# Optimization experiments

Hardware: AMD Instinct MI355X
Metric: run time of the kernel (lower is better)

## Reference

```python
import jax, jax.numpy as jnp
import numpy as np
from functools import partial

EMB = 768
ATTN = 768
HEADS = 12
N = 4096
K = 64
ALPHA = 0.5
TEMP = 0.5
THRESH = 1e-4
MAX_ITER = 100
DKM_EPS = 1e-6
LN_EPS = 1e-5


def setup_inputs() -> dict:
    key = jax.random.key(0)
    ks = jax.random.split(key, 12)
    s = 0.02
    return {
        "original_embeddings": jax.random.normal(ks[0], (N, EMB), jnp.float32),
        "fc1_w": jax.random.normal(ks[1], (ATTN, EMB), jnp.float32) * s,
        "fc1_b": jnp.zeros((ATTN,), jnp.float32),
        "fc2_w": jax.random.normal(ks[2], (EMB, ATTN), jnp.float32) * s,
        "fc2_b": jnp.zeros((EMB,), jnp.float32),
        "in_proj_w": jax.random.normal(ks[3], (3 * ATTN, ATTN), jnp.float32) * s,
        "in_proj_b": jnp.zeros((3 * ATTN,), jnp.float32),
        "out_w": jax.random.normal(ks[4], (ATTN, ATTN), jnp.float32) * s,
        "out_b": jnp.zeros((ATTN,), jnp.float32),
        "ln_g": jnp.ones((EMB,), jnp.float32),
        "ln_b": jnp.zeros((EMB,), jnp.float32),
        "init_idx": jax.random.randint(ks[5], (K,), 0, N, jnp.int64 if jax.config.jax_enable_x64 else jnp.int32),
        "k_cl": K,
    }


def _cdist(x, c):
    # squared euclidean via expansion, clipped for numerical safety
    sq = (jnp.sum(x * x, 1)[:, None] + jnp.sum(c * c, 1)[None, :]
          - 2.0 * (x @ c.T))
    return jnp.sqrt(jnp.maximum(sq, 0.0))


def _dkm_step(X, C):
    a = jax.nn.softmax(-_cdist(X, C) / TEMP, axis=1)   # [N, K]
    a_sum = jnp.sum(a, axis=0) + DKM_EPS               # [K]
    C_new = (a.T @ X) / a_sum[:, None]                 # [K, D]
    return a, C_new


def _transform(x, fc1_w, fc1_b, fc2_w, fc2_b, in_proj_w, in_proj_b, out_w, out_b, ln_g, ln_b):
    h = jax.nn.relu(x @ fc1_w.T + fc1_b)               # [N, A]
    qkv = h @ in_proj_w.T + in_proj_b                  # [N, 3A]
    q, k, v = jnp.split(qkv, 3, axis=1)
    hd = ATTN // HEADS
    q = q.reshape(N, HEADS, hd).transpose(1, 0, 2)     # [H, N, hd]
    k = k.reshape(N, HEADS, hd).transpose(1, 0, 2)
    v = v.reshape(N, HEADS, hd).transpose(1, 0, 2)
    scores = jnp.einsum('hnd,hmd->hnm', q, k) / np.sqrt(hd).astype(np.float32)
    attn = jax.nn.softmax(scores, axis=-1)             # [H, N, N]
    o = jnp.einsum('hnm,hmd->hnd', attn, v)            # [H, N, hd]
    o = o.transpose(1, 0, 2).reshape(N, ATTN)
    o = o @ out_w.T + out_b
    y = jax.nn.relu(o @ fc2_w.T + fc2_b)               # [N, E]
    z = (1.0 - ALPHA) * x + ALPHA * y
    mu = jnp.mean(z, axis=-1, keepdims=True)
    var = jnp.mean((z - mu) ** 2, axis=-1, keepdims=True)
    return (z - mu) / jnp.sqrt(var + LN_EPS) * ln_g + ln_b


def reference(original_embeddings, fc1_w, fc1_b, fc2_w, fc2_b,
              in_proj_w, in_proj_b, out_w, out_b, ln_g, ln_b,
              init_idx, k_cl):
    X = _transform(original_embeddings, fc1_w, fc1_b, fc2_w, fc2_b,
                   in_proj_w, in_proj_b, out_w, out_b, ln_g, ln_b)
    C0 = X[init_idx]                                   # [K, E]
    a0, C1 = _dkm_step(X, C0)
    diff0 = jnp.sum(jnp.abs(C1 - C0))

    def cond(st):
        _, _, _, diff, i = st
        return (diff > THRESH) & (i < MAX_ITER)

    def body(st):
        _, _, C_new, _, i = st
        C = C_new
        a, C_new2 = _dkm_step(X, C)
        diff = jnp.sum(jnp.abs(C_new2 - C))
        return (C, a, C_new2, diff, i + 1)

    C, a, _, _, _ = jax.lax.while_loop(cond, body, (C0, a0, C1, diff0, jnp.int32(0)))
    return C, a
```

## Files before the change

### kernel.cpp

```cpp
#include <hip/hip_runtime.h>
#include <cstdint>

typedef __bf16 bf16;
typedef __bf16 bf16x4 __attribute__((ext_vector_type(4)));
typedef __bf16 bf16x8 __attribute__((ext_vector_type(8)));
typedef float  f32x4  __attribute__((ext_vector_type(4)));

#define LOG2E 1.44269504088896340736f

__device__ __forceinline__ f32x4 mfma16(bf16x8 a, bf16x8 b, f32x4 c) {
  return __builtin_amdgcn_mfma_f32_16x16x32_bf16(a, b, c, 0, 0, 0);
}

__device__ __forceinline__ void gl2lds16(const bf16* g, bf16* l) {
  __builtin_amdgcn_global_load_lds(
      (const __attribute__((address_space(1))) unsigned int*)g,
      (__attribute__((address_space(3))) unsigned int*)l, 16, 0, 0);
}

__global__ __launch_bounds__(256) void cvt_all(
    const float* __restrict__ x0, const float* __restrict__ w1,
    const float* __restrict__ w2, const float* __restrict__ wip,
    const float* __restrict__ wo,
    bf16* __restrict__ dx0, bf16* __restrict__ dw1, bf16* __restrict__ dw2,
    bf16* __restrict__ dwip, bf16* __restrict__ dwo, float* __restrict__ ctrl)
{
  int i = blockIdx.x * 256 + threadIdx.x;
  if (blockIdx.x == 0) {
    for (int u = threadIdx.x; u < 8192; u += 256) ctrl[u] = 0.f;
  }
  const float* s; bf16* d; int base;
  if      (i <  786432) { s = x0;  d = dx0;  base = 0; }
  else if (i <  933888) { s = w1;  d = dw1;  base = 786432; }
  else if (i < 1081344) { s = w2;  d = dw2;  base = 933888; }
  else if (i < 1523712) { s = wip; d = dwip; base = 1081344; }
  else                  { s = wo;  d = dwo;  base = 1523712; }
  int j = i - base;
  f32x4 v = ((const f32x4*)s)[j];
  bf16x4 r;
  r[0] = (bf16)v[0]; r[1] = (bf16)v[1]; r[2] = (bf16)v[2]; r[3] = (bf16)v[3];
  ((bf16x4*)d)[j] = r;
}

template<int RELU, int OUTF32>
__global__ __launch_bounds__(256) void gemm128(
    const bf16* __restrict__ A, const bf16* __restrict__ W,
    const float* __restrict__ bias, bf16* __restrict__ outb,
    float* __restrict__ outf, int N)
{
  __shared__ bf16 Ab[2][8192];
  __shared__ bf16 Bb[2][8192];
  const int tid = threadIdx.x;
  const int w = tid >> 6, lane = tid & 63;
  const int q2 = lane >> 4, c = lane & 15;
  const int wrow = (w >> 1) * 64, wcol = (w & 1) * 64;
  const int mb = blockIdx.x * 128, nb = blockIdx.y * 128;
  const int srow = tid >> 3, sgrp = tid & 7;

  auto stage = [&](const bf16* __restrict__ src, int rowbase, int kb, bf16* dst) {
#pragma unroll
    for (int i = 0; i < 4; ++i) {
      int row = i * 32 + srow;
      int gs = (sgrp ^ (row & 7)) * 8;
      gl2lds16(src + (size_t)(rowbase + row) * 768 + kb + gs,
               dst + i * 2048 + tid * 8);
    }
  };

  f32x4 acc[4][4] = {};
  stage(A, mb, 0, Ab[0]);
  stage(W, nb, 0, Bb[0]);
  for (int kb = 0; kb < 12; ++kb) {
    const int buf = kb & 1;
    __syncthreads();
    if (kb < 11) {
      stage(A, mb, (kb + 1) * 64, Ab[buf ^ 1]);
      stage(W, nb, (kb + 1) * 64, Bb[buf ^ 1]);
    }
#pragma unroll
    for (int kc = 0; kc < 2; ++kc) {
      bf16x8 af[4], bfr[4];
#pragma unroll
      for (int rt = 0; rt < 4; ++rt) {
        int r = wrow + rt * 16 + c;
        af[rt] = *(const bf16x8*)&Ab[buf][r * 64 + (((kc * 4 + q2) ^ (r & 7)) * 8)];
      }
#pragma unroll
      for (int ct = 0; ct < 4; ++ct) {
        int r = wcol + ct * 16 + c;
        bfr[ct] = *(const bf16x8*)&Bb[buf][r * 64 + (((kc * 4 + q2) ^ (r & 7)) * 8)];
      }
#pragma unroll
      for (int rt = 0; rt < 4; ++rt)
#pragma unroll
        for (int ct = 0; ct < 4; ++ct)
          acc[rt][ct] = mfma16(af[rt], bfr[ct], acc[rt][ct]);
    }
  }
#pragma unroll
  for (int rt = 0; rt < 4; ++rt) {
#pragma unroll
    for (int ct = 0; ct < 4; ++ct) {
      int col = nb + wcol + ct * 16 + c;
      float bv = bias[col];
#pragma unroll
      for (int j = 0; j < 4; ++j) {
        int row = mb + wrow + rt * 16 + q2 * 4 + j;
        float v = acc[rt][ct][j] + bv;
        if (RELU) v = fmaxf(v, 0.f);
        if (OUTF32) outf[(size_t)row * N + col] = v;
        else        outb[(size_t)row * N + col] = (bf16)v;
      }
    }
  }
}

__global__ __launch_bounds__(256) void transpose_bf16(
    const bf16* __restrict__ src, bf16* __restrict__ dst, int stride, int colOff)
{
  __shared__ bf16 t[64][72];
  const int br = blockIdx.x, bc = blockIdx.y;
  {
    int ir = threadIdx.x >> 2, icb = (threadIdx.x & 3) * 16;
    const bf16* srow = src + (size_t)(br * 64 + ir) * stride + colOff + bc * 64 + icb;
    *(bf16x8*)&t[ir][icb] = *(const bf16x8*)srow;
    *(bf16x8*)&t[ir][icb + 8] = *(const bf16x8*)(srow + 8);
  }
  __syncthreads();
  {
    int oc = threadIdx.x >> 2, orb = (threadIdx.x & 3) * 16;
    bf16x8 v0, v1;
#pragma unroll
    for (int j = 0; j < 8; ++j) { v0[j] = t[orb + j][oc]; v1[j] = t[orb + 8 + j][oc]; }
    bf16* drow = dst + (size_t)(bc * 64 + oc) * 4096 + br * 64 + orb;
    *(bf16x8*)drow = v0;
    *(bf16x8*)(drow + 8) = v1;
  }
}

__global__ __launch_bounds__(256) void attn_kernel(
    const bf16* __restrict__ qkv, const bf16* __restrict__ vt, bf16* __restrict__ o)
{
  const int h = blockIdx.x >> 6;
  const int qt = blockIdx.x & 63;
  const int w = threadIdx.x >> 6, lane = threadIdx.x & 63;
  const int q2 = lane >> 4, c = lane & 15;
  const int qbase = qt * 64 + w * 16;
  __shared__ bf16 Ks[2][64][64];
  __shared__ bf16 Vs[2][64][64];
  __shared__ bf16 Pl[4][16][72];

  const bf16* Qr = qkv + (size_t)(qbase + c) * 2304 + h * 64 + q2 * 8;
  bf16x8 a0 = *(const bf16x8*)(Qr);
  bf16x8 a1 = *(const bf16x8*)(Qr + 32);

  const int srow = lane >> 3;
  const int sg = ((lane & 7) ^ srow) * 8;
  const bf16* kg = qkv + (size_t)(w * 16 + srow) * 2304 + 768 + h * 64 + sg;
  const bf16* vg = vt + (size_t)(h * 64 + w * 16 + srow) * 4096 + sg;

  auto stage = [&](int jt, int buf) {
    const int kvb = jt * 64;
    gl2lds16(kg + (size_t)kvb * 2304,       &Ks[buf][w * 16][0]);
    gl2lds16(kg + (size_t)(kvb + 8) * 2304, &Ks[buf][w * 16 + 8][0]);
    gl2lds16(vg + kvb,                      &Vs[buf][w * 16][0]);
    gl2lds16(vg + kvb + 8 * 4096,           &Vs[buf][w * 16 + 8][0]);
  };

  bf16x8 ones;
#pragma unroll
  for (int i = 0; i < 8; ++i) ones[i] = (bf16)1.0f;

  f32x4 oa[4] = {};
  f32x4 accl = {};
  const int gsw = (q2 ^ (c & 7)) * 8;
  const float SC = 0.125f * LOG2E;

  stage(0, 0);
  for (int jt = 0; jt < 64; ++jt) {
    const int buf = jt & 1;
    __syncthreads();
    if (jt < 63) stage(jt + 1, buf ^ 1);
    f32x4 s[4];
#pragma unroll
    for (int nt = 0; nt < 4; ++nt) {
      const int row = nt * 16 + c;
      bf16x8 b0 = *(const bf16x8*)&Ks[buf][row][gsw];
      bf16x8 b1 = *(const bf16x8*)&Ks[buf][row][gsw ^ 32];
      f32x4 t = {};
      t = mfma16(a0, b0, t);
      t = mfma16(a1, b1, t);
      s[nt] = t;
    }
#pragma unroll
    for (int nt = 0; nt < 4; ++nt)
#pragma unroll
      for (int j = 0; j < 4; ++j)
        Pl[w][q2 * 4 + j][nt * 16 + c] = (bf16)exp2f(s[nt][j] * SC);
    bf16x8 p0 = *(const bf16x8*)(&Pl[w][c][q2 * 8]);
    bf16x8 p1 = *(const bf16x8*)(&Pl[w][c][32 + q2 * 8]);
    accl = mfma16(p0, ones, accl);
    accl = mfma16(p1, ones, accl);
#pragma unroll
    for (int dt = 0; dt < 4; ++dt) {
      const int row = dt * 16 + c;
      bf16x8 v0 = *(const bf16x8*)&Vs[buf][row][gsw];
      bf16x8 v1 = *(const bf16x8*)&Vs[buf][row][gsw ^ 32];
      oa[dt] = mfma16(p0, v0, oa[dt]);
      oa[dt] = mfma16(p1, v1, oa[dt]);
    }
  }
#pragma unroll
  for (int dt = 0; dt < 4; ++dt)
#pragma unroll
    for (int j = 0; j < 4; ++j) {
      int row = qbase + q2 * 4 + j;
      int col = h * 64 + dt * 16 + c;
      o[(size_t)row * 768 + col] = (bf16)(oa[dt][j] / accl[j]);
    }
}

__global__ __launch_bounds__(256) void ln_kernel(
    const float* __restrict__ x0, const float* __restrict__ y,
    const float* __restrict__ g, const float* __restrict__ b,
    float* __restrict__ X, bf16* __restrict__ Xb, float* __restrict__ xn2)
{
  const int w = threadIdx.x >> 6, lane = threadIdx.x & 63;
  const int row = blockIdx.x * 4 + w;
  const float* xr = x0 + (size_t)row * 768;
  const float* yr = y + (size_t)row * 768;
  float z[12]; float s = 0.f;
#pragma unroll
  for (int i = 0; i < 12; ++i) {
    int col = lane + i * 64;
    float zz = 0.5f * xr[col] + 0.5f * yr[col];
    z[i] = zz; s += zz;
  }
#pragma unroll
  for (int off = 32; off; off >>= 1) s += __shfl_xor(s, off, 64);
  float mu = s * (1.f / 768.f);
  float v = 0.f;
#pragma unroll
  for (int i = 0; i < 12; ++i) { float d = z[i] - mu; v += d * d; }
#pragma unroll
  for (int off = 32; off; off >>= 1) v += __shfl_xor(v, off, 64);
  float rstd = rsqrtf(v * (1.f / 768.f) + 1e-5f);
  float sn = 0.f;
#pragma unroll
  for (int i = 0; i < 12; ++i) {
    int col = lane + i * 64;
    float xv = (z[i] - mu) * rstd * g[col] + b[col];
    X[(size_t)row * 768 + col] = xv;
    Xb[(size_t)row * 768 + col] = (bf16)xv;
    sn += xv * xv;
  }
#pragma unroll
  for (int off = 32; off; off >>= 1) sn += __shfl_xor(sn, off, 64);
  if (lane == 0) xn2[row] = sn;
}

__device__ __forceinline__ void gridbar(int* bar, int& ep, int g) {
  __syncthreads();
  if (threadIdx.x == 0) {
    ep++;
    __builtin_amdgcn_fence(__ATOMIC_RELEASE, "agent");
    int v = __hip_atomic_fetch_add(bar + g * 64, 1, __ATOMIC_RELAXED,
                                   __HIP_MEMORY_SCOPE_AGENT) + 1;
    if (v == 32 * ep) {
      int tv = __hip_atomic_fetch_add(bar + 512, 1, __ATOMIC_RELAXED,
                                      __HIP_MEMORY_SCOPE_AGENT) + 1;
      if (tv == 8 * ep) {
#pragma unroll
        for (int i = 0; i < 8; ++i)
          __hip_atomic_store(bar + 1024 + i * 64, ep, __ATOMIC_RELAXED,
                             __HIP_MEMORY_SCOPE_AGENT);
      }
    }
    long guard = 0;
    while (__hip_atomic_load(bar + 1024 + g * 64, __ATOMIC_RELAXED,
                             __HIP_MEMORY_SCOPE_AGENT) < ep) {
      __builtin_amdgcn_s_sleep(2);
      if (++guard > (1L << 28)) break;
    }
    __builtin_amdgcn_fence(__ATOMIC_ACQUIRE, "agent");
  }
  __syncthreads();
}

__global__ __launch_bounds__(256) void dkm_fused(
    const float* __restrict__ XF, const int* __restrict__ idx,
    const bf16* __restrict__ Xb, const bf16* __restrict__ Xt,
    const float* __restrict__ xn2,
    float* __restrict__ CB, bf16* __restrict__ CBH,
    bf16* __restrict__ aT, float* __restrict__ a_out, float* __restrict__ outC,
    float* __restrict__ asumall, float* __restrict__ cnall,
    float* __restrict__ diffall, int* __restrict__ bar)
{
  extern __shared__ char dynsmem[];
  bf16* XtL = (bf16*)dynsmem;
  __shared__ bf16 XL[16][776];
  __shared__ float GsRed[1024];
  __shared__ float asl[64];
  __shared__ float cnl[16];
  __shared__ float dred[4];
  __shared__ float sdiff;
  float (*Gs)[64] = (float(*)[64])GsRed;
  float (*red)[16][16] = (float(*)[16][16])GsRed;
  const int tid = threadIdx.x;
  const int w = tid >> 6, lane = tid & 63;
  const int q2 = lane >> 4, c = lane & 15;
  const int b = blockIdx.x;
  const int g = b & 7;
  const int rbase = b * 16;
  const int tr = b / 48, tc = b % 48;
  int ep = 0;

  {
    int row = tid >> 4, seg = (tid & 15) * 48;
    const bf16* src = Xb + (size_t)(rbase + row) * 768 + seg;
#pragma unroll
    for (int i = 0; i < 6; ++i)
      *(bf16x8*)&XL[row][seg + i * 8] = *(const bf16x8*)(src + i * 8);
  }
  if (b < 192) {
    const int row = tid >> 4, cc = tid & 15;
    const bf16* XtS = Xt + (size_t)(tc * 16 + row) * 4096;
#pragma unroll
    for (int i = 0; i < 32; ++i) {
      int gg = i * 16 + cc;
      bf16x8 vv = *(const bf16x8*)(XtS + gg * 8);
      *(bf16x8*)&XtL[(size_t)row * 4096 + ((gg ^ (row & 7)) * 8)] = vv;
    }
  }
  if (b < 64) {
    const int src = idx[b];
    float s = 0.f;
#pragma unroll
    for (int u = 0; u < 3; ++u) {
      int d = u * 256 + tid;
      float v = XF[(size_t)src * 768 + d];
      CB[(size_t)b * 768 + d] = v;
      CBH[(size_t)b * 768 + d] = (bf16)v;
      s += v * v;
    }
#pragma unroll
    for (int off = 32; off; off >>= 1) s += __shfl_xor(s, off, 64);
    if (lane == 0) dred[w] = s;
    __syncthreads();
    if (tid == 0) cnall[b] = dred[0] + dred[1] + dred[2] + dred[3];
  }
  const int arow = tid >> 4, aci = tid & 15;
  const float xn = xn2[rbase + arow];
  gridbar(bar, ep, g);

  int p = 0;
  for (int t = 0; t < 100; ++t) {
    const int par = t & 1;
    {
      if (b == 0) {
        if (tid >= 128 && tid < 192) asumall[(par ^ 1) * 64 + tid - 128] = 0.f;
        else if (tid >= 192)         cnall[(par ^ 1) * 64 + tid - 192] = 0.f;
      }
      const bf16* C = CBH + (size_t)par * 49152;
      const float* cnp = cnall + par * 64;
      f32x4 acc = {};
      const bf16* Cr = C + (size_t)(w * 16 + c) * 768 + q2 * 8;
#pragma unroll
      for (int ks = 0; ks < 24; ++ks) {
        bf16x8 a = *(const bf16x8*)&XL[c][q2 * 8 + ks * 32];
        bf16x8 bb = *(const bf16x8*)(Cr + ks * 32);
        acc = mfma16(a, bb, acc);
      }
      if (tid < 64) asl[tid] = 0.f;
#pragma unroll
      for (int j = 0; j < 4; ++j) Gs[q2 * 4 + j][w * 16 + c] = acc[j];
      __syncthreads();
      float lg[4];
#pragma unroll
      for (int u = 0; u < 4; ++u) {
        int col = aci + u * 16;
        float d2 = xn + cnp[col] - 2.f * Gs[arow][col];
        lg[u] = -2.f * sqrtf(fmaxf(d2, 0.f));
      }
      float mx = fmaxf(fmaxf(lg[0], lg[1]), fmaxf(lg[2], lg[3]));
#pragma unroll
      for (int off = 8; off; off >>= 1) mx = fmaxf(mx, __shfl_xor(mx, off, 16));
      float sum = 0.f;
#pragma unroll
      for (int u = 0; u < 4; ++u) { float e = exp2f((lg[u] - mx) * LOG2E); lg[u] = e; sum += e; }
#pragma unroll
      for (int off = 8; off; off >>= 1) sum += __shfl_xor(sum, off, 16);
      float rs = 1.f / sum;
#pragma unroll
      for (int u = 0; u < 4; ++u) {
        int col = aci + u * 16;
        float av = lg[u] * rs;
        aT[(size_t)col * 4096 + rbase + arow] = (bf16)av;
        atomicAdd(&asl[col], av);
      }
      __syncthreads();
      if (tid < 64) atomicAdd(&asumall[par * 64 + tid], asl[tid]);
    }
    gridbar(bar, ep, g);
    if (b < 192) {
      f32x4 acc = {};
      const bf16* Ar = aT + (size_t)(tr * 16 + c) * 4096 + q2 * 8;
#pragma unroll 4
      for (int i = 0; i < 32; ++i) {
        int kb = (w + i * 4) * 32;
        int gb = (w + i * 4) * 4 + q2;
        bf16x8 bv = *(const bf16x8*)&XtL[(size_t)c * 4096 + ((gb ^ (c & 7)) * 8)];
        acc = mfma16(*(const bf16x8*)(Ar + kb), bv, acc);
      }
#pragma unroll
      for (int j = 0; j < 4; ++j) red[w][q2 * 4 + j][c] = acc[j];
      if (tid < 16) cnl[tid] = 0.f;
      __syncthreads();
      const int r = tid >> 4, cl = tid & 15;
      float s = red[0][r][cl] + red[1][r][cl] + red[2][r][cl] + red[3][r][cl];
      const int cluster = tr * 16 + r, dcol = tc * 16 + cl;
      float denom = asumall[par * 64 + cluster] + 1e-6f;
      float cnew = s / denom;
      size_t cidx = (size_t)cluster * 768 + dcol;
      float cold = CB[(size_t)par * 49152 + cidx];
      CB[(size_t)(par ^ 1) * 49152 + cidx] = cnew;
      CBH[(size_t)(par ^ 1) * 49152 + cidx] = (bf16)cnew;
      atomicAdd(&cnl[r], cnew * cnew);
      float dv = fabsf(cnew - cold);
#pragma unroll
      for (int off = 32; off; off >>= 1) dv += __shfl_xor(dv, off, 64);
      if (lane == 0) dred[w] = dv;
      __syncthreads();
      if (tid < 16)
        atomicAdd(&cnall[(par ^ 1) * 64 + tr * 16 + tid], cnl[tid]);
      if (tid == 0)
        atomicAdd(&diffall[par], dred[0] + dred[1] + dred[2] + dred[3]);
    } else if (b == 255 && tid == 0) {
      diffall[par ^ 1] = 0.f;
    }
    gridbar(bar, ep, g);
    if (tid == 0)
      sdiff = *(volatile const float*)&diffall[par];
    __syncthreads();
    if (sdiff <= 1e-4f) { p = par; break; }
    p = (t + 1) & 1;
  }
  {
    const bf16* C = CBH + (size_t)p * 49152;
    const float* cnp = cnall + p * 64;
    f32x4 acc = {};
    const bf16* Cr = C + (size_t)(w * 16 + c) * 768 + q2 * 8;
#pragma unroll
    for (int ks = 0; ks < 24; ++ks) {
      bf16x8 a = *(const bf16x8*)&XL[c][q2 * 8 + ks * 32];
      bf16x8 bb = *(const bf16x8*)(Cr + ks * 32);
      acc = mfma16(a, bb, acc);
    }
    __syncthreads();
#pragma unroll
    for (int j = 0; j < 4; ++j) Gs[q2 * 4 + j][w * 16 + c] = acc[j];
    __syncthreads();
    float lg[4];
#pragma unroll
    for (int u = 0; u < 4; ++u) {
      int col = aci + u * 16;
      float d2 = xn + cnp[col] - 2.f * Gs[arow][col];
      lg[u] = -2.f * sqrtf(fmaxf(d2, 0.f));
    }
    float mx = fmaxf(fmaxf(lg[0], lg[1]), fmaxf(lg[2], lg[3]));
#pragma unroll
    for (int off = 8; off; off >>= 1) mx = fmaxf(mx, __shfl_xor(mx, off, 16));
    float sum = 0.f;
#pragma unroll
    for (int u = 0; u < 4; ++u) { float e = exp2f((lg[u] - mx) * LOG2E); lg[u] = e; sum += e; }
#pragma unroll
    for (int off = 8; off; off >>= 1) sum += __shfl_xor(sum, off, 16);
    float rs = 1.f / sum;
#pragma unroll
    for (int u = 0; u < 4; ++u)
      a_out[(size_t)(rbase + arow) * 64 + aci + u * 16] = lg[u] * rs;
  }
  if (tid < 192) outC[b * 192 + tid] = CB[(size_t)p * 49152 + b * 192 + tid];
}

extern "C" void kernel_launch(void* const* d_in, const int* in_sizes, int n_in,
                              void* d_out, int out_size, void* d_ws, size_t ws_size,
                              hipStream_t stream) {
  const float* x0   = (const float*)d_in[0];
  const float* fc1w = (const float*)d_in[1];
  const float* fc1b = (const float*)d_in[2];
  const float* fc2w = (const float*)d_in[3];
  const float* fc2b = (const float*)d_in[4];
  const float* ipw  = (const float*)d_in[5];
  const float* ipb  = (const float*)d_in[6];
  const float* outw = (const float*)d_in[7];
  const float* outbias = (const float*)d_in[8];
  const float* lng  = (const float*)d_in[9];
  const float* lnb  = (const float*)d_in[10];
  const int*   idx  = (const int*)d_in[11];

  char* p = (char*)d_ws;
  auto take = [&](size_t n) { char* r = p; p += (n + 255) & ~(size_t)255; return r; };
  bf16* X0B   = (bf16*)take((size_t)4096 * 768 * 2);
  bf16* W1B   = (bf16*)take((size_t)768 * 768 * 2);
  bf16* FC2WB = (bf16*)take((size_t)768 * 768 * 2);
  bf16* IPWB  = (bf16*)take((size_t)2304 * 768 * 2);
  bf16* OUTWB = (bf16*)take((size_t)768 * 768 * 2);
  bf16* HB    = (bf16*)take((size_t)4096 * 768 * 2);
  bf16* QKVB  = (bf16*)take((size_t)4096 * 2304 * 2);
  bf16* VT    = (bf16*)take((size_t)768 * 4096 * 2);
  bf16* OB    = (bf16*)take((size_t)4096 * 768 * 2);
  bf16* O2B   = (bf16*)take((size_t)4096 * 768 * 2);
  float* YF   = (float*)take((size_t)4096 * 768 * 4);
  float* XF   = (float*)take((size_t)4096 * 768 * 4);
  bf16* XBB   = (bf16*)take((size_t)4096 * 768 * 2);
  bf16* XTB   = (bf16*)take((size_t)768 * 4096 * 2);
  float* XN2  = (float*)take((size_t)4096 * 4);
  float* CB   = (float*)take((size_t)2 * 49152 * 4);
  bf16* CBH   = (bf16*)take((size_t)2 * 49152 * 2);
  bf16* ATB   = (bf16*)take((size_t)64 * 4096 * 2);
  float* CTRLF = (float*)take(8192 * 4);
  float* ASUM = CTRLF;
  float* CN   = CTRLF + 128;
  float* DIFF = CTRLF + 256;
  int* BAR    = (int*)(CTRLF + 512);

  float* aout = (float*)d_out + 49152;

  cvt_all<<<6528, 256, 0, stream>>>(x0, fc1w, fc2w, ipw, outw,
                                    X0B, W1B, FC2WB, IPWB, OUTWB, CTRLF);
  gemm128<1, 0><<<dim3(32, 6), 256, 0, stream>>>(X0B, W1B, fc1b, HB, nullptr, 768);
  gemm128<0, 0><<<dim3(32, 18), 256, 0, stream>>>(HB, IPWB, ipb, QKVB, nullptr, 2304);
  transpose_bf16<<<dim3(64, 12), 256, 0, stream>>>(QKVB, VT, 2304, 1536);
  attn_kernel<<<768, 256, 0, stream>>>(QKVB, VT, OB);
  gemm128<0, 0><<<dim3(32, 6), 256, 0, stream>>>(OB, OUTWB, outbias, O2B, nullptr, 768);
  gemm128<1, 1><<<dim3(32, 6), 256, 0, stream>>>(O2B, FC2WB, fc2b, nullptr, YF, 768);
  ln_kernel<<<1024, 256, 0, stream>>>(x0, YF, lng, lnb, XF, XBB, XN2);
  transpose_bf16<<<dim3(64, 12), 256, 0, stream>>>(XBB, XTB, 768, 0);
  dkm_fused<<<256, 256, 131072, stream>>>(XF, idx, XBB, XTB, XN2, CB, CBH, ATB, aout,
                                          (float*)d_out, ASUM, CN, DIFF, BAR);
}
```

Measured before the change: 562.0 us.

## Fold out-proj into fc2 weights, widen attention KV tiles, split DKM accumulators

Precomputes the product of the fc2 and out-projection weights, plus a combined bias, so that one GEMM replaces two per-token GEMMs after attention. The attention kernel now stages 128-key tiles per iteration, halving the number of barriers and stage calls, with a new swizzle for the V tile. The DKM distance and centroid MFMA chains are split into four independent accumulators to shorten dependency chains. The folded weight product adds small setup kernels and an extra bf16 rounding of the combined weight, which may slightly change numerics.

```diff
diff --git a/kernel.cpp b/kernel.cpp
--- a/kernel.cpp
+++ b/kernel.cpp
@@ -42,6 +42,16 @@
   ((bf16x4*)d)[j] = r;
 }
 
+__global__ __launch_bounds__(256) void bias_fuse(
+    const float* __restrict__ w2, const float* __restrict__ bo,
+    const float* __restrict__ b2, float* __restrict__ bc)
+{
+  int n = blockIdx.x * 256 + threadIdx.x;
+  float s = 0.f;
+  for (int j = 0; j < 768; ++j) s += w2[(size_t)n * 768 + j] * bo[j];
+  bc[n] = b2[n] + s;
+}
+
 template<int RELU, int OUTF32>
 __global__ __launch_bounds__(256) void gemm128(
     const bf16* __restrict__ A, const bf16* __restrict__ W,
@@ -116,7 +126,8 @@
 }
 
 __global__ __launch_bounds__(256) void transpose_bf16(
-    const bf16* __restrict__ src, bf16* __restrict__ dst, int stride, int colOff)
+    const bf16* __restrict__ src, bf16* __restrict__ dst,
+    int stride, int colOff, int dstride)
 {
   __shared__ bf16 t[64][72];
   const int br = blockIdx.x, bc = blockIdx.y;
@@ -132,7 +143,7 @@
     bf16x8 v0, v1;
 #pragma unroll
     for (int j = 0; j < 8; ++j) { v0[j] = t[orb + j][oc]; v1[j] = t[orb + 8 + j][oc]; }
-    bf16* drow = dst + (size_t)(bc * 64 + oc) * 4096 + br * 64 + orb;
+    bf16* drow = dst + (size_t)(bc * 64 + oc) * dstride + br * 64 + orb;
     *(bf16x8*)drow = v0;
     *(bf16x8*)(drow + 8) = v1;
   }
@@ -146,25 +157,33 @@
   const int w = threadIdx.x >> 6, lane = threadIdx.x & 63;
   const int q2 = lane >> 4, c = lane & 15;
   const int qbase = qt * 64 + w * 16;
-  __shared__ bf16 Ks[2][64][64];
-  __shared__ bf16 Vs[2][64][64];
+  __shared__ bf16 Ks[2][128][64];
+  __shared__ bf16 Vs[2][64][128];
   __shared__ bf16 Pl[4][16][72];
 
   const bf16* Qr = qkv + (size_t)(qbase + c) * 2304 + h * 64 + q2 * 8;
   bf16x8 a0 = *(const bf16x8*)(Qr);
   bf16x8 a1 = *(const bf16x8*)(Qr + 32);
 
-  const int srow = lane >> 3;
-  const int sg = ((lane & 7) ^ srow) * 8;
-  const bf16* kg = qkv + (size_t)(w * 16 + srow) * 2304 + 768 + h * 64 + sg;
-  const bf16* vg = vt + (size_t)(h * 64 + w * 16 + srow) * 4096 + sg;
+  const int sr8 = lane >> 3, sc8 = lane & 7;
+  const int sr4 = lane >> 4, sc16 = lane & 15;
+  const int kcol = ((sc8 ^ sr8) * 8);
 
   auto stage = [&](int jt, int buf) {
-    const int kvb = jt * 64;
-    gl2lds16(kg + (size_t)kvb * 2304,       &Ks[buf][w * 16][0]);
-    gl2lds16(kg + (size_t)(kvb + 8) * 2304, &Ks[buf][w * 16 + 8][0]);
-    gl2lds16(vg + kvb,                      &Vs[buf][w * 16][0]);
-    gl2lds16(vg + kvb + 8 * 4096,           &Vs[buf][w * 16 + 8][0]);
+    const int kvb = jt * 128;
+#pragma unroll
+    for (int i = 0; i < 4; ++i) {
+      int rb = w * 32 + i * 8;
+      gl2lds16(qkv + (size_t)(kvb + rb + sr8) * 2304 + 768 + h * 64 + kcol,
+               &Ks[buf][rb][0]);
+    }
+#pragma unroll
+    for (int i = 0; i < 4; ++i) {
+      int rb = w * 16 + i * 4;
+      int key = i * 4 + sr4;
+      gl2lds16(vt + (size_t)(h * 64 + rb + sr4) * 4096 + kvb + (sc16 ^ key) * 8,
+               &Vs[buf][rb][0]);
+    }
   };
 
   bf16x8 ones;
@@ -177,37 +196,41 @@
   const float SC = 0.125f * LOG2E;
 
   stage(0, 0);
-  for (int jt = 0; jt < 64; ++jt) {
+  for (int jt = 0; jt < 32; ++jt) {
     const int buf = jt & 1;
     __syncthreads();
-    if (jt < 63) stage(jt + 1, buf ^ 1);
-    f32x4 s[4];
-#pragma unroll
-    for (int nt = 0; nt < 4; ++nt) {
-      const int row = nt * 16 + c;
-      bf16x8 b0 = *(const bf16x8*)&Ks[buf][row][gsw];
-      bf16x8 b1 = *(const bf16x8*)&Ks[buf][row][gsw ^ 32];
-      f32x4 t = {};
-      t = mfma16(a0, b0, t);
-      t = mfma16(a1, b1, t);
-      s[nt] = t;
-    }
-#pragma unroll
-    for (int nt = 0; nt < 4; ++nt)
-#pragma unroll
-      for (int j = 0; j < 4; ++j)
-        Pl[w][q2 * 4 + j][nt * 16 + c] = (bf16)exp2f(s[nt][j] * SC);
-    bf16x8 p0 = *(const bf16x8*)(&Pl[w][c][q2 * 8]);
-    bf16x8 p1 = *(const bf16x8*)(&Pl[w][c][32 + q2 * 8]);
-    accl = mfma16(p0, ones, accl);
-    accl = mfma16(p1, ones, accl);
-#pragma unroll
-    for (int dt = 0; dt < 4; ++dt) {
-      const int row = dt * 16 + c;
-      bf16x8 v0 = *(const bf16x8*)&Vs[buf][row][gsw];
-      bf16x8 v1 = *(const bf16x8*)&Vs[buf][row][gsw ^ 32];
-      oa[dt] = mfma16(p0, v0, oa[dt]);
-      oa[dt] = mfma16(p1, v1, oa[dt]);
+    if (jt < 31) stage(jt + 1, buf ^ 1);
+#pragma unroll
+    for (int half = 0; half < 2; ++half) {
+      f32x4 s[4];
+#pragma unroll
+      for (int nt = 0; nt < 4; ++nt) {
+        const int row = half * 64 + nt * 16 + c;
+        bf16x8 b0 = *(const bf16x8*)&Ks[buf][row][gsw];
+        bf16x8 b1 = *(const bf16x8*)&Ks[buf][row][gsw ^ 32];
+        f32x4 t = {};
+        t = mfma16(a0, b0, t);
+        t = mfma16(a1, b1, t);
+        s[nt] = t;
+      }
+#pragma unroll
+      for (int nt = 0; nt < 4; ++nt)
+#pragma unroll
+        for (int j = 0; j < 4; ++j)
+          Pl[w][q2 * 4 + j][nt * 16 + c] = (bf16)exp2f(s[nt][j] * SC);
+      bf16x8 p0 = *(const bf16x8*)(&Pl[w][c][q2 * 8]);
+      bf16x8 p1 = *(const bf16x8*)(&Pl[w][c][32 + q2 * 8]);
+      accl = mfma16(p0, ones, accl);
+      accl = mfma16(p1, ones, accl);
+      const int G0 = half * 8 + q2;
+#pragma unroll
+      for (int dt = 0; dt < 4; ++dt) {
+        const int row = dt * 16 + c;
+        bf16x8 v0 = *(const bf16x8*)&Vs[buf][row][(G0 ^ c) * 8];
+        bf16x8 v1 = *(const bf16x8*)&Vs[buf][row][((G0 + 4) ^ c) * 8];
+        oa[dt] = mfma16(p0, v0, oa[dt]);
+        oa[dt] = mfma16(p1, v1, oa[dt]);
+      }
     }
   }
 #pragma unroll
@@ -363,14 +386,20 @@
       }
       const bf16* C = CBH + (size_t)par * 49152;
       const float* cnp = cnall + par * 64;
-      f32x4 acc = {};
       const bf16* Cr = C + (size_t)(w * 16 + c) * 768 + q2 * 8;
-#pragma unroll
-      for (int ks = 0; ks < 24; ++ks) {
-        bf16x8 a = *(const bf16x8*)&XL[c][q2 * 8 + ks * 32];
-        bf16x8 bb = *(const bf16x8*)(Cr + ks * 32);
-        acc = mfma16(a, bb, acc);
-      }
+      f32x4 a0 = {}, a1 = {}, a2 = {}, a3 = {};
+#pragma unroll
+      for (int ks = 0; ks < 24; ks += 4) {
+        a0 = mfma16(*(const bf16x8*)&XL[c][q2 * 8 + ks * 32],
+                    *(const bf16x8*)(Cr + ks * 32), a0);
+        a1 = mfma16(*(const bf16x8*)&XL[c][q2 * 8 + (ks + 1) * 32],
+                    *(const bf16x8*)(Cr + (ks + 1) * 32), a1);
+        a2 = mfma16(*(const bf16x8*)&XL[c][q2 * 8 + (ks + 2) * 32],
+                    *(const bf16x8*)(Cr + (ks + 2) * 32), a2);
+        a3 = mfma16(*(const bf16x8*)&XL[c][q2 * 8 + (ks + 3) * 32],
+                    *(const bf16x8*)(Cr + (ks + 3) * 32), a3);
+      }
+      f32x4 acc = (a0 + a1) + (a2 + a3);
       if (tid < 64) asl[tid] = 0.f;
 #pragma unroll
       for (int j = 0; j < 4; ++j) Gs[q2 * 4 + j][w * 16 + c] = acc[j];
@@ -403,15 +432,24 @@
     }
     gridbar(bar, ep, g);
     if (b < 192) {
-      f32x4 acc = {};
       const bf16* Ar = aT + (size_t)(tr * 16 + c) * 4096 + q2 * 8;
-#pragma unroll 4
-      for (int i = 0; i < 32; ++i) {
-        int kb = (w + i * 4) * 32;
-        int gb = (w + i * 4) * 4 + q2;
-        bf16x8 bv = *(const bf16x8*)&XtL[(size_t)c * 4096 + ((gb ^ (c & 7)) * 8)];
-        acc = mfma16(*(const bf16x8*)(Ar + kb), bv, acc);
-      }
+      f32x4 b0 = {}, b1 = {}, b2 = {}, b3 = {};
+#pragma unroll
+      for (int i = 0; i < 32; i += 4) {
+#pragma unroll
+        for (int u = 0; u < 4; ++u) {
+          int ii = i + u;
+          int kb = (w + ii * 4) * 32;
+          int gb = (w + ii * 4) * 4 + q2;
+          bf16x8 bv = *(const bf16x8*)&XtL[(size_t)c * 4096 + ((gb ^ (c & 7)) * 8)];
+          bf16x8 av = *(const bf16x8*)(Ar + kb);
+          if (u == 0) b0 = mfma16(av, bv, b0);
+          else if (u == 1) b1 = mfma16(av, bv, b1);
+          else if (u == 2) b2 = mfma16(av, bv, b2);
+          else b3 = mfma16(av, bv, b3);
+        }
+      }
+      f32x4 acc = (b0 + b1) + (b2 + b3);
 #pragma unroll
       for (int j = 0; j < 4; ++j) red[w][q2 * 4 + j][c] = acc[j];
       if (tid < 16) cnl[tid] = 0.f;
@@ -506,11 +544,13 @@
   bf16* FC2WB = (bf16*)take((size_t)768 * 768 * 2);
   bf16* IPWB  = (bf16*)take((size_t)2304 * 768 * 2);
   bf16* OUTWB = (bf16*)take((size_t)768 * 768 * 2);
+  bf16* WOT   = (bf16*)take((size_t)768 * 768 * 2);
+  bf16* WCB   = (bf16*)take((size_t)768 * 768 * 2);
+  float* BC   = (float*)take(768 * 4);
   bf16* HB    = (bf16*)take((size_t)4096 * 768 * 2);
   bf16* QKVB  = (bf16*)take((size_t)4096 * 2304 * 2);
   bf16* VT    = (bf16*)take((size_t)768 * 4096 * 2);
   bf16* OB    = (bf16*)take((size_t)4096 * 768 * 2);
-  bf16* O2B   = (bf16*)take((size_t)4096 * 768 * 2);
   float* YF   = (float*)take((size_t)4096 * 768 * 4);
   float* XF   = (float*)take((size_t)4096 * 768 * 4);
   bf16* XBB   = (bf16*)take((size_t)4096 * 768 * 2);
@@ -524,19 +564,23 @@
   float* CN   = CTRLF + 128;
   float* DIFF = CTRLF + 256;
   int* BAR    = (int*)(CTRLF + 512);
+  float* ZB   = CTRLF + 4096;
 
   float* aout = (float*)d_out + 49152;
 
   cvt_all<<<6528, 256, 0, stream>>>(x0, fc1w, fc2w, ipw, outw,
                                     X0B, W1B, FC2WB, IPWB, OUTWB, CTRLF);
+  transpose_bf16<<<dim3(12, 12), 256, 0, stream>>>(OUTWB, WOT, 768, 0, 768);
+  bias_fuse<<<3, 256, 0, stream>>>(fc2w, outbias, fc2b, BC);
+  gemm128<0, 0><<<dim3(6, 6), 256, 0, stream>>>(FC2WB, WOT, ZB, WCB, nullptr, 768);
+
   gemm128<1, 0><<<dim3(32, 6), 256, 0, stream>>>(X0B, W1B, fc1b, HB, nullptr, 768);
   gemm128<0, 0><<<dim3(32, 18), 256, 0, stream>>>(HB, IPWB, ipb, QKVB, nullptr, 2304);
-  transpose_bf16<<<dim3(64, 12), 256, 0, stream>>>(QKVB, VT, 2304, 1536);
+  transpose_bf16<<<dim3(64, 12), 256, 0, stream>>>(QKVB, VT, 2304, 1536, 4096);
   attn_kernel<<<768, 256, 0, stream>>>(QKVB, VT, OB);
-  gemm128<0, 0><<<dim3(32, 6), 256, 0, stream>>>(OB, OUTWB, outbias, O2B, nullptr, 768);
-  gemm128<1, 1><<<dim3(32, 6), 256, 0, stream>>>(O2B, FC2WB, fc2b, nullptr, YF, 768);
+  gemm128<1, 1><<<dim3(32, 6), 256, 0, stream>>>(OB, WCB, BC, nullptr, YF, 768);
   ln_kernel<<<1024, 256, 0, stream>>>(x0, YF, lng, lnb, XF, XBB, XN2);
-  transpose_bf16<<<dim3(64, 12), 256, 0, stream>>>(XBB, XTB, 768, 0);
+  transpose_bf16<<<dim3(64, 12), 256, 0, stream>>>(XBB, XTB, 768, 0, 4096);
   dkm_fused<<<256, 256, 131072, stream>>>(XF, idx, XBB, XTB, XN2, CB, CBH, ATB, aout,
                                           (float*)d_out, ASUM, CN, DIFF, BAR);
 }
```

New measurement: 595.7 us. +6.0%, slower.
